# Kernel optimization log

Hardware: AMD Instinct MI355X
Metric: run time of the kernel (lower is better)

Reference implementation:

```python
import jax, jax.numpy as jnp
import numpy as np

B, C, H, W = 8, 256, 64, 64
S = 2            # area_size = sqrt(num_areas)
A = S * S        # num_areas
NH = 8           # num_heads (hardcoded in module)
EPS = 1e-5       # nn.LayerNorm default eps


def setup_inputs() -> dict:
    key = jax.random.key(0)
    ks = jax.random.split(key, 4)
    scale = 0.02
    return {
        "x": jax.random.normal(ks[0], (B, C, H, W), jnp.float32),
        "W_in": jax.random.normal(ks[1], (A, 3 * C, C), jnp.float32) * scale,
        "b_in": jnp.zeros((A, 3 * C), jnp.float32),
        "W_out": jax.random.normal(ks[2], (A, C, C), jnp.float32) * scale,
        "b_out": jnp.zeros((A, C), jnp.float32),
        "gamma": jnp.ones((C,), jnp.float32),
        "beta": jnp.zeros((C,), jnp.float32),
    }


def reference(x, W_in, b_in, W_out, b_out, gamma, beta):
    b, c, h, w = x.shape
    ah, aw = h // S, w // S
    L = ah * aw
    dh = c // NH

    # split into 2x2 areas, flatten each to a sequence: [B, A, L, C]
    # area index = i*S + j (row-major), matching the torch loop order
    xa = (x.reshape(b, c, S, ah, S, aw)
            .transpose(0, 2, 4, 3, 5, 1)   # [B, i, j, ah, aw, C]
            .reshape(b, A, L, c))

    # per-area in-projection (torch Linear: y = x @ W^T + b)
    qkv = jnp.einsum('balc,adc->bald', xa, W_in) + b_in[None, :, None, :]
    q, k, v = jnp.split(qkv, 3, axis=-1)
    q = q.reshape(b, A, L, NH, dh)
    k = k.reshape(b, A, L, NH, dh)
    v = v.reshape(b, A, L, NH, dh)

    scale = jnp.asarray(dh, x.dtype) ** -0.5
    scores = jnp.einsum('balhd,bamhd->bahlm', q * scale, k)  # [B,A,NH,L,L]
    attn = jax.nn.softmax(scores, axis=-1)
    o = jnp.einsum('bahlm,bamhd->balhd', attn, v).reshape(b, A, L, c)
    o = jnp.einsum('balc,adc->bald', o, W_out) + b_out[None, :, None, :]

    # residual + shared LayerNorm over channel dim
    y = o + xa
    mu = jnp.mean(y, axis=-1, keepdims=True)
    var = jnp.mean((y - mu) ** 2, axis=-1, keepdims=True)
    y = (y - mu) * jax.lax.rsqrt(var + EPS) * gamma + beta

    # reassemble areas back to [B, C, H, W]
    out = (y.reshape(b, S, S, ah, aw, c)
             .transpose(0, 5, 1, 3, 2, 4)  # [B, C, i, ah, j, aw]
             .reshape(b, c, h, w))
    return out
```

## Files before the change

### kernel.cpp

```cpp
#include <hip/hip_runtime.h>
#include <cstdint>
#include <cstddef>

#define B_    8
#define C_    256
#define H_    64
#define W_    64
#define A_    4
#define NH_   8
#define DH_   32
#define L_    1024
#define NPAIR 32
#define QKVN  768

typedef __bf16 bf16;
typedef __bf16 bf16x8 __attribute__((ext_vector_type(8)));
typedef __bf16 bf16x4 __attribute__((ext_vector_type(4)));
typedef float  f32x4  __attribute__((ext_vector_type(4)));

#define QSCALE 0.25506866729736328f

__device__ inline f32x4 mfma16(bf16x8 a, bf16x8 b, f32x4 c) {
    return __builtin_amdgcn_mfma_f32_16x16x32_bf16(a, b, c, 0, 0, 0);
}
__device__ inline bf16x8 ld8(const bf16* p) { return *(const bf16x8*)p; }

__device__ inline void stage16(const bf16* g, bf16* l) {
    __builtin_amdgcn_global_load_lds(
        (const __attribute__((address_space(1))) void*)g,
        (__attribute__((address_space(3))) void*)l, 16, 0, 0);
}

#define NW4 (786432 / 4)
#define NO4 (262144 / 4)
__global__ __launch_bounds__(256) void k_split(const float* __restrict__ x,
                                               bf16* __restrict__ xa,
                                               const float* __restrict__ Win,
                                               const float* __restrict__ Wout,
                                               bf16* __restrict__ Winb,
                                               bf16* __restrict__ Woutb) {
    __shared__ float lds[32][257];
    int bid = blockIdx.x;
    int t = threadIdx.x;
    if (bid >= NPAIR * 32) {
        int tid = (bid - NPAIR * 32) * 256 + t;
        if (tid < NW4) {
            float4 v = ((const float4*)Win)[tid];
            bf16x4 ov = {(bf16)v.x, (bf16)v.y, (bf16)v.z, (bf16)v.w};
            ((bf16x4*)Winb)[tid] = ov;
        } else if (tid < NW4 + NO4) {
            int t2 = tid - NW4;
            float4 v = ((const float4*)Wout)[t2];
            bf16x4 ov = {(bf16)v.x, (bf16)v.y, (bf16)v.z, (bf16)v.w};
            ((bf16x4*)Woutb)[t2] = ov;
        }
        return;
    }
    int pair = bid >> 5, p = bid & 31;
    int b = pair >> 2, a = pair & 3, i = a >> 1, j = a & 1;
    int q = t & 31, csub = t >> 5;
    const float* xb = x + (size_t)b * C_ * H_ * W_ + (size_t)(i * 32 + p) * W_ + j * 32;
    for (int r = 0; r < 32; ++r) {
        int c = r * 8 + csub;
        lds[q][c] = xb[(size_t)c * H_ * W_ + q];
    }
    __syncthreads();
    bf16* xr = xa + ((size_t)pair * L_ + (size_t)p * 32) * C_;
    for (int r = 0; r < 32; ++r) {
        xr[(size_t)r * C_ + t] = (bf16)lds[r][t];
    }
}

__global__ __launch_bounds__(256) void k_qkv(const bf16* __restrict__ xa,
                                             const bf16* __restrict__ Win,
                                             const float* __restrict__ bin,
                                             bf16* __restrict__ qk,
                                             bf16* __restrict__ vT) {
    __shared__ __align__(16) bf16 lA[128 * 64];
    __shared__ __align__(16) bf16 lB[128 * 64];
    int bid = blockIdx.x;
    int nt = bid % 6, mt = (bid / 6) & 7, pair = bid / 48;
    int a = pair & 3;
    int t = threadIdx.x, w = t >> 6, lane = t & 63;
    int wm = w >> 1, wn = w & 1;
    int quad = lane >> 4, l16 = lane & 15;
    int m0 = mt * 128, n0 = nt * 128;
    int r8 = lane >> 3, pc = lane & 7, jj = pc ^ r8;
    const bf16* ga = xa + (size_t)pair * L_ * C_ + (size_t)(m0 + w * 32 + r8) * C_ + jj * 8;
    const bf16* gb = Win + (size_t)a * QKVN * C_ + (size_t)(n0 + w * 32 + r8) * C_ + jj * 8;
    f32x4 acc[4][4];
#pragma unroll
    for (int fm = 0; fm < 4; ++fm)
#pragma unroll
        for (int fn = 0; fn < 4; ++fn) acc[fm][fn] = (f32x4){0.f, 0.f, 0.f, 0.f};
    for (int k0 = 0; k0 < C_; k0 += 64) {
        __syncthreads();
#pragma unroll
        for (int i = 0; i < 4; ++i) {
            stage16(ga + (size_t)(i * 8) * C_ + k0, lA + (w * 32 + i * 8) * 64);
            stage16(gb + (size_t)(i * 8) * C_ + k0, lB + (w * 32 + i * 8) * 64);
        }
        __syncthreads();
#pragma unroll
        for (int ks = 0; ks < 2; ++ks) {
            int p = (ks * 4 + quad) ^ (l16 & 7);
            bf16x8 am[4], bn[4];
#pragma unroll
            for (int f = 0; f < 4; ++f) {
                am[f] = *(const bf16x8*)&lA[(wm * 64 + f * 16 + l16) * 64 + p * 8];
                bn[f] = *(const bf16x8*)&lB[(wn * 64 + f * 16 + l16) * 64 + p * 8];
            }
#pragma unroll
            for (int fm = 0; fm < 4; ++fm)
#pragma unroll
                for (int fn = 0; fn < 4; ++fn)
                    acc[fm][fn] = mfma16(am[fm], bn[fn], acc[fm][fn]);
        }
    }
    int colbase = n0 + wn * 64;
    int mb = m0 + wm * 64;
    if (colbase < 512) {
        float sc = (colbase < 256) ? QSCALE : 1.0f;
        bf16* ob = qk + (size_t)pair * L_ * 512;
#pragma unroll
        for (int fn = 0; fn < 4; ++fn) {
            int col = colbase + fn * 16 + l16;
            float bias = bin[a * QKVN + col];
#pragma unroll
            for (int fm = 0; fm < 4; ++fm) {
                int m = mb + fm * 16 + quad * 4;
#pragma unroll
                for (int r = 0; r < 4; ++r)
                    ob[(size_t)(m + r) * 512 + col] = (bf16)((acc[fm][fn][r] + bias) * sc);
            }
        }
    } else {
        bf16* vb = vT + (size_t)pair * C_ * L_;
#pragma unroll
        for (int fn = 0; fn < 4; ++fn) {
            int e = colbase - 512 + fn * 16 + l16;
            float bias = bin[a * QKVN + colbase + fn * 16 + l16];
#pragma unroll
            for (int fm = 0; fm < 4; ++fm) {
                int m = mb + fm * 16 + quad * 4;
                bf16x4 pk = {(bf16)(acc[fm][fn][0] + bias), (bf16)(acc[fm][fn][1] + bias),
                             (bf16)(acc[fm][fn][2] + bias), (bf16)(acc[fm][fn][3] + bias)};
                *(bf16x4*)&vb[(size_t)e * L_ + m] = pk;
            }
        }
    }
}

__global__ __launch_bounds__(256) void k_attn(const bf16* __restrict__ qk,
                                              const bf16* __restrict__ vT,
                                              bf16* __restrict__ o) {
    __shared__ __align__(16) bf16 pl[4][4][16 * 72];
    int bid = blockIdx.x;
    int pair = bid & 31, rest = bid >> 5;
    int head = rest & 7, qb = rest >> 3;
    int t = threadIdx.x, w = t >> 6, lane = t & 63, quad = lane >> 4, l16 = lane & 15;
    const bf16* qbp  = qk + (size_t)pair * L_ * 512;
    const bf16* kptr = qbp + 256 + head * DH_ + quad * 8;
    const bf16* vt0  = vT + ((size_t)pair * C_ + head * DH_) * L_;
    int qbase = qb * 256 + w * 64;
    bf16x8 qf[4];
    f32x4 acc0[4], acc1[4], l4[4];
#pragma unroll
    for (int f = 0; f < 4; ++f) {
        qf[f] = ld8(qbp + (size_t)(qbase + f * 16 + l16) * 512 + head * DH_ + quad * 8);
        acc0[f] = (f32x4){0.f, 0.f, 0.f, 0.f};
        acc1[f] = (f32x4){0.f, 0.f, 0.f, 0.f};
        l4[f]   = (f32x4){0.f, 0.f, 0.f, 0.f};
    }
    for (int kv0 = 0; kv0 < L_; kv0 += 64) {
        bf16x8 kf[4], vf[4];
#pragma unroll
        for (int kb = 0; kb < 4; ++kb)
            kf[kb] = ld8(kptr + (size_t)(kv0 + l16 * 4 + kb) * 512);
#pragma unroll
        for (int ks = 0; ks < 2; ++ks) {
            vf[ks * 2 + 0] = ld8(vt0 + (size_t)l16 * L_ + kv0 + ks * 32 + quad * 8);
            vf[ks * 2 + 1] = ld8(vt0 + (size_t)(16 + l16) * L_ + kv0 + ks * 32 + quad * 8);
        }
#pragma unroll
        for (int f = 0; f < 4; ++f) {
            f32x4 s[4];
#pragma unroll
            for (int kb = 0; kb < 4; ++kb) s[kb] = mfma16(qf[f], kf[kb], (f32x4){0.f, 0.f, 0.f, 0.f});
            bf16* pw = &pl[w][f][0];
#pragma unroll
            for (int r = 0; r < 4; ++r) {
                float p0 = __builtin_amdgcn_exp2f(s[0][r]);
                float p1 = __builtin_amdgcn_exp2f(s[1][r]);
                float p2 = __builtin_amdgcn_exp2f(s[2][r]);
                float p3 = __builtin_amdgcn_exp2f(s[3][r]);
                l4[f][r] += (p0 + p1) + (p2 + p3);
                bf16x4 pv = {(bf16)p0, (bf16)p1, (bf16)p2, (bf16)p3};
                *(bf16x4*)&pw[(quad * 4 + r) * 72 + l16 * 4] = pv;
            }
#pragma unroll
            for (int ks = 0; ks < 2; ++ks) {
                bf16x8 pf = *(const bf16x8*)&pw[l16 * 72 + ks * 32 + quad * 8];
                acc0[f] = mfma16(pf, vf[ks * 2 + 0], acc0[f]);
                acc1[f] = mfma16(pf, vf[ks * 2 + 1], acc1[f]);
            }
        }
    }
    bf16* orow = o + (size_t)pair * L_ * C_ + head * DH_;
#pragma unroll
    for (int f = 0; f < 4; ++f) {
#pragma unroll
        for (int r = 0; r < 4; ++r) {
            float s1 = l4[f][r];
#pragma unroll
            for (int off = 1; off < 16; off <<= 1) s1 += __shfl_xor(s1, off);
            float inv = 1.f / s1;
            int row = qbase + f * 16 + quad * 4 + r;
            orow[(size_t)row * C_ + l16]      = (bf16)(acc0[f][r] * inv);
            orow[(size_t)row * C_ + 16 + l16] = (bf16)(acc1[f][r] * inv);
        }
    }
}

__global__ __launch_bounds__(256) void k_out(const bf16* __restrict__ o,
                                             const bf16* __restrict__ Wout,
                                             const float* __restrict__ bout,
                                             const bf16* __restrict__ xa,
                                             const float* __restrict__ gamma,
                                             const float* __restrict__ beta,
                                             bf16* __restrict__ y) {
    __shared__ __align__(16) bf16 lA[128 * 64];
    __shared__ __align__(16) bf16 lB[256 * 64];
    __shared__ float red[2][2][64][2];
    int bid = blockIdx.x;
    int mt = bid & 7, pair = bid >> 3;
    int a = pair & 3;
    int t = threadIdx.x, w = t >> 6, lane = t & 63;
    int wm = w >> 1, wn = w & 1;
    int quad = lane >> 4, l16 = lane & 15;
    int m0 = mt * 128;
    int r8 = lane >> 3, pc = lane & 7, jj = pc ^ r8;
    const bf16* ga = o + (size_t)pair * L_ * C_ + (size_t)(m0 + w * 32 + r8) * C_ + jj * 8;
    const bf16* gb = Wout + (size_t)a * C_ * C_ + (size_t)(w * 64 + r8) * C_ + jj * 8;
    f32x4 acc[4][8];
#pragma unroll
    for (int fm = 0; fm < 4; ++fm)
#pragma unroll
        for (int fn = 0; fn < 8; ++fn) acc[fm][fn] = (f32x4){0.f, 0.f, 0.f, 0.f};
    for (int k0 = 0; k0 < C_; k0 += 64) {
        __syncthreads();
#pragma unroll
        for (int i = 0; i < 4; ++i)
            stage16(ga + (size_t)(i * 8) * C_ + k0, lA + (w * 32 + i * 8) * 64);
#pragma unroll
        for (int i = 0; i < 8; ++i)
            stage16(gb + (size_t)(i * 8) * C_ + k0, lB + (w * 64 + i * 8) * 64);
        __syncthreads();
#pragma unroll
        for (int ks = 0; ks < 2; ++ks) {
            int p = (ks * 4 + quad) ^ (l16 & 7);
            bf16x8 am[4], bn[8];
#pragma unroll
            for (int f = 0; f < 4; ++f)
                am[f] = *(const bf16x8*)&lA[(wm * 64 + f * 16 + l16) * 64 + p * 8];
#pragma unroll
            for (int f = 0; f < 8; ++f)
                bn[f] = *(const bf16x8*)&lB[(wn * 128 + f * 16 + l16) * 64 + p * 8];
#pragma unroll
            for (int fm = 0; fm < 4; ++fm)
#pragma unroll
                for (int fn = 0; fn < 8; ++fn)
                    acc[fm][fn] = mfma16(am[fm], bn[fn], acc[fm][fn]);
        }
    }
    const bf16* xb = xa + ((size_t)pair * L_ + m0 + wm * 64) * C_;
#pragma unroll
    for (int fn = 0; fn < 8; ++fn) {
        int col = wn * 128 + fn * 16 + l16;
        float bias = bout[a * C_ + col];
#pragma unroll
        for (int fm = 0; fm < 4; ++fm)
#pragma unroll
            for (int r = 0; r < 4; ++r)
                acc[fm][fn][r] += bias + (float)xb[(size_t)(fm * 16 + quad * 4 + r) * C_ + col];
    }
#pragma unroll
    for (int fm = 0; fm < 4; ++fm) {
#pragma unroll
        for (int r = 0; r < 4; ++r) {
            float s1 = 0.f, s2 = 0.f;
#pragma unroll
            for (int fn = 0; fn < 8; ++fn) {
                float v = acc[fm][fn][r];
                s1 += v; s2 += v * v;
            }
#pragma unroll
            for (int off = 1; off < 16; off <<= 1) {
                s1 += __shfl_xor(s1, off);
                s2 += __shfl_xor(s2, off);
            }
            if (l16 == 0) {
                int rl = fm * 16 + quad * 4 + r;
                red[wm][wn][rl][0] = s1;
                red[wm][wn][rl][1] = s2;
            }
        }
    }
    __syncthreads();
    bf16* yb = y + ((size_t)pair * L_ + m0 + wm * 64) * C_;
#pragma unroll
    for (int fm = 0; fm < 4; ++fm) {
#pragma unroll
        for (int r = 0; r < 4; ++r) {
            int rl = fm * 16 + quad * 4 + r;
            float t1 = red[wm][0][rl][0] + red[wm][1][rl][0];
            float t2 = red[wm][0][rl][1] + red[wm][1][rl][1];
            float mu = t1 * (1.f / 256.f);
            float var = t2 * (1.f / 256.f) - mu * mu;
            float rstd = rsqrtf(var + 1e-5f);
#pragma unroll
            for (int fn = 0; fn < 8; ++fn) {
                int col = wn * 128 + fn * 16 + l16;
                yb[(size_t)rl * C_ + col] =
                    (bf16)((acc[fm][fn][r] - mu) * rstd * gamma[col] + beta[col]);
            }
        }
    }
}

__global__ __launch_bounds__(256) void k_merge(const bf16* __restrict__ y,
                                               float* __restrict__ out) {
    __shared__ float lds[32][257];
    int bid = blockIdx.x;
    int pair = bid >> 5, p = bid & 31;
    int b = pair >> 2, a = pair & 3, i = a >> 1, j = a & 1;
    int t = threadIdx.x;
    int q = t & 31, csub = t >> 5;
    const bf16* yr = y + ((size_t)pair * L_ + (size_t)p * 32) * C_;
    for (int r = 0; r < 32; ++r) {
        lds[r][t] = (float)yr[(size_t)r * C_ + t];
    }
    __syncthreads();
    float* xb = out + (size_t)b * C_ * H_ * W_ + (size_t)(i * 32 + p) * W_ + j * 32;
    for (int r = 0; r < 32; ++r) {
        int c = r * 8 + csub;
        xb[(size_t)c * H_ * W_ + q] = lds[q][c];
    }
}

extern "C" void kernel_launch(void* const* d_in, const int* in_sizes, int n_in,
                              void* d_out, int out_size, void* d_ws, size_t ws_size,
                              hipStream_t stream) {
    (void)in_sizes; (void)n_in; (void)out_size; (void)ws_size;
    const float* x     = (const float*)d_in[0];
    const float* Win   = (const float*)d_in[1];
    const float* bin   = (const float*)d_in[2];
    const float* Wout  = (const float*)d_in[3];
    const float* bout  = (const float*)d_in[4];
    const float* gamma = (const float*)d_in[5];
    const float* beta  = (const float*)d_in[6];
    float* out = (float*)d_out;

    char* ws = (char*)d_ws;
    bf16* xa    = (bf16*)ws;
    bf16* qk    = (bf16*)(ws + ((size_t)16 << 20));
    bf16* vT    = (bf16*)(ws + ((size_t)48 << 20));
    bf16* o     = (bf16*)(ws + ((size_t)64 << 20));
    bf16* Winb  = (bf16*)(ws + ((size_t)80 << 20));
    bf16* Woutb = (bf16*)(ws + ((size_t)82 << 20));
    bf16* y     = (bf16*)(ws + ((size_t)16 << 20));

    k_split<<<NPAIR * 32 + 1024, 256, 0, stream>>>(x, xa, Win, Wout, Winb, Woutb);
    k_qkv<<<NPAIR * 8 * 6, 256, 0, stream>>>(xa, Winb, bin, qk, vT);
    k_attn<<<NPAIR * NH_ * 4, 256, 0, stream>>>(qk, vT, o);
    k_out<<<NPAIR * 8, 256, 0, stream>>>(o, Woutb, bout, xa, gamma, beta, y);
    k_merge<<<NPAIR * 32, 256, 0, stream>>>(y, out);
}
```

Baseline: 225.7 us.

## Prefetch next K tile, split QK/exp and PV phases with sched barriers and priority

Restructures the attention inner loop. The K fragments for the next 64-key tile are now loaded after the QK/exp phase of the current tile, so the load overlaps the PV MFMAs. The QK+exp work for all four query fragments is grouped ahead of the PV MFMAs, with sched_barrier and setprio hints to order MFMA issue, and launch_bounds now requests 4 blocks per CU. The aim is to hide global load latency. In exchange it adds register pressure from the prefetched fragments and constrains the compiler's scheduling.

Measured after the change: 393.6 us. 1.74x slower.

```diff
diff --git a/kernel.cpp b/kernel.cpp
--- a/kernel.cpp
+++ b/kernel.cpp
@@ -151,9 +151,9 @@
     }
 }
 
-__global__ __launch_bounds__(256) void k_attn(const bf16* __restrict__ qk,
-                                              const bf16* __restrict__ vT,
-                                              bf16* __restrict__ o) {
+__global__ __launch_bounds__(256, 4) void k_attn(const bf16* __restrict__ qk,
+                                                 const bf16* __restrict__ vT,
+                                                 bf16* __restrict__ o) {
     __shared__ __align__(16) bf16 pl[4][4][16 * 72];
     int bid = blockIdx.x;
     int pair = bid & 31, rest = bid >> 5;
@@ -172,39 +172,61 @@
         acc1[f] = (f32x4){0.f, 0.f, 0.f, 0.f};
         l4[f]   = (f32x4){0.f, 0.f, 0.f, 0.f};
     }
+    bf16x8 ka[4], va[4];
+#pragma unroll
+    for (int kb = 0; kb < 4; ++kb)
+        ka[kb] = ld8(kptr + (size_t)(l16 * 4 + kb) * 512);
+
     for (int kv0 = 0; kv0 < L_; kv0 += 64) {
-        bf16x8 kf[4], vf[4];
-#pragma unroll
-        for (int kb = 0; kb < 4; ++kb)
-            kf[kb] = ld8(kptr + (size_t)(kv0 + l16 * 4 + kb) * 512);
 #pragma unroll
         for (int ks = 0; ks < 2; ++ks) {
-            vf[ks * 2 + 0] = ld8(vt0 + (size_t)l16 * L_ + kv0 + ks * 32 + quad * 8);
-            vf[ks * 2 + 1] = ld8(vt0 + (size_t)(16 + l16) * L_ + kv0 + ks * 32 + quad * 8);
-        }
+            va[ks * 2 + 0] = ld8(vt0 + (size_t)l16 * L_ + kv0 + ks * 32 + quad * 8);
+            va[ks * 2 + 1] = ld8(vt0 + (size_t)(16 + l16) * L_ + kv0 + ks * 32 + quad * 8);
+        }
+        __builtin_amdgcn_sched_barrier(0);
 #pragma unroll
         for (int f = 0; f < 4; ++f) {
             f32x4 s[4];
-#pragma unroll
-            for (int kb = 0; kb < 4; ++kb) s[kb] = mfma16(qf[f], kf[kb], (f32x4){0.f, 0.f, 0.f, 0.f});
+            __builtin_amdgcn_s_setprio(1);
+#pragma unroll
+            for (int kb = 0; kb < 4; ++kb)
+                s[kb] = mfma16(qf[f], ka[kb], (f32x4){0.f, 0.f, 0.f, 0.f});
+            __builtin_amdgcn_s_setprio(0);
+            f32x4 e0, e1, e2, e3;
+#pragma unroll
+            for (int r = 0; r < 4; ++r) {
+                e0[r] = __builtin_amdgcn_exp2f(s[0][r]);
+                e1[r] = __builtin_amdgcn_exp2f(s[1][r]);
+                e2[r] = __builtin_amdgcn_exp2f(s[2][r]);
+                e3[r] = __builtin_amdgcn_exp2f(s[3][r]);
+            }
+            l4[f] += (e0 + e1) + (e2 + e3);
             bf16* pw = &pl[w][f][0];
 #pragma unroll
             for (int r = 0; r < 4; ++r) {
-                float p0 = __builtin_amdgcn_exp2f(s[0][r]);
-                float p1 = __builtin_amdgcn_exp2f(s[1][r]);
-                float p2 = __builtin_amdgcn_exp2f(s[2][r]);
-                float p3 = __builtin_amdgcn_exp2f(s[3][r]);
-                l4[f][r] += (p0 + p1) + (p2 + p3);
-                bf16x4 pv = {(bf16)p0, (bf16)p1, (bf16)p2, (bf16)p3};
+                bf16x4 pv = {(bf16)e0[r], (bf16)e1[r], (bf16)e2[r], (bf16)e3[r]};
                 *(bf16x4*)&pw[(quad * 4 + r) * 72 + l16 * 4] = pv;
             }
+        }
+        __builtin_amdgcn_sched_barrier(0);
+        if (kv0 + 64 < L_) {
+#pragma unroll
+            for (int kb = 0; kb < 4; ++kb)
+                ka[kb] = ld8(kptr + (size_t)(kv0 + 64 + l16 * 4 + kb) * 512);
+        }
+        __builtin_amdgcn_sched_barrier(0);
+        __builtin_amdgcn_s_setprio(1);
+#pragma unroll
+        for (int f = 0; f < 4; ++f) {
+            const bf16* pw = &pl[w][f][0];
 #pragma unroll
             for (int ks = 0; ks < 2; ++ks) {
                 bf16x8 pf = *(const bf16x8*)&pw[l16 * 72 + ks * 32 + quad * 8];
-                acc0[f] = mfma16(pf, vf[ks * 2 + 0], acc0[f]);
-                acc1[f] = mfma16(pf, vf[ks * 2 + 1], acc1[f]);
-            }
-        }
+                acc0[f] = mfma16(pf, va[ks * 2 + 0], acc0[f]);
+                acc1[f] = mfma16(pf, va[ks * 2 + 1], acc1[f]);
+            }
+        }
+        __builtin_amdgcn_s_setprio(0);
     }
     bf16* orow = o + (size_t)pair * L_ * C_ + head * DH_;
 #pragma unroll
```

## Stage shared K/V tiles in LDS with prefetch and swizzle P buffer

Applied to the files above, without the earlier changes.

The attention kernel now loads each 64-key K and V tile cooperatively into LDS once per block instead of every wave issuing its own redundant global loads. The next tile is prefetched right after the current one is read into registers, with block-wide barriers around the loop. The P scratch buffer changes from a padded layout to an XOR-swizzled one to avoid bank conflicts. Together these aim to cut global memory traffic and LDS conflicts, at the cost of two __syncthreads per iteration and extra LDS use that may lower occupancy.

New measurement: 212.1 us. 1.06x faster.

```diff
diff --git a/kernel.cpp b/kernel.cpp
--- a/kernel.cpp
+++ b/kernel.cpp
@@ -154,14 +154,19 @@
 __global__ __launch_bounds__(256) void k_attn(const bf16* __restrict__ qk,
                                               const bf16* __restrict__ vT,
                                               bf16* __restrict__ o) {
-    __shared__ __align__(16) bf16 pl[4][4][16 * 72];
+    __shared__ __align__(16) bf16 pl[4][4][1024];
+    __shared__ __align__(16) bf16 klds[4 * 512];
+    __shared__ __align__(16) bf16 vlds[4 * 512];
     int bid = blockIdx.x;
     int pair = bid & 31, rest = bid >> 5;
     int head = rest & 7, qb = rest >> 3;
     int t = threadIdx.x, w = t >> 6, lane = t & 63, quad = lane >> 4, l16 = lane & 15;
-    const bf16* qbp  = qk + (size_t)pair * L_ * 512;
-    const bf16* kptr = qbp + 256 + head * DH_ + quad * 8;
-    const bf16* vt0  = vT + ((size_t)pair * C_ + head * DH_) * L_;
+    const bf16* qbp = qk + (size_t)pair * L_ * 512;
+    const bf16* kg = qbp + (size_t)(l16 * 4 + w) * 512 + 256 + head * DH_ + quad * 8;
+    const bf16* vg = vT + ((size_t)pair * C_ + head * DH_ + (w & 1) * 16 + l16) * L_
+                        + (w >> 1) * 32 + quad * 8;
+    bf16* kdst = &klds[w * 512];
+    bf16* vdst = &vlds[w * 512];
     int qbase = qb * 256 + w * 64;
     bf16x8 qf[4];
     f32x4 acc0[4], acc1[4], l4[4];
@@ -172,22 +177,28 @@
         acc1[f] = (f32x4){0.f, 0.f, 0.f, 0.f};
         l4[f]   = (f32x4){0.f, 0.f, 0.f, 0.f};
     }
+    stage16(kg, kdst);
+    stage16(vg, vdst);
+    __syncthreads();
+
     for (int kv0 = 0; kv0 < L_; kv0 += 64) {
         bf16x8 kf[4], vf[4];
 #pragma unroll
-        for (int kb = 0; kb < 4; ++kb)
-            kf[kb] = ld8(kptr + (size_t)(kv0 + l16 * 4 + kb) * 512);
-#pragma unroll
-        for (int ks = 0; ks < 2; ++ks) {
-            vf[ks * 2 + 0] = ld8(vt0 + (size_t)l16 * L_ + kv0 + ks * 32 + quad * 8);
-            vf[ks * 2 + 1] = ld8(vt0 + (size_t)(16 + l16) * L_ + kv0 + ks * 32 + quad * 8);
-        }
+        for (int i = 0; i < 4; ++i) {
+            kf[i] = ld8(&klds[(i * 64 + lane) * 8]);
+            vf[i] = ld8(&vlds[(i * 64 + lane) * 8]);
+        }
+        __syncthreads();
+        int kvn = (kv0 + 64) & (L_ - 1);
+        stage16(kg + (size_t)kvn * 512, kdst);
+        stage16(vg + kvn, vdst);
 #pragma unroll
         for (int f = 0; f < 4; ++f) {
             f32x4 s[4];
 #pragma unroll
-            for (int kb = 0; kb < 4; ++kb) s[kb] = mfma16(qf[f], kf[kb], (f32x4){0.f, 0.f, 0.f, 0.f});
-            bf16* pw = &pl[w][f][0];
+            for (int kb = 0; kb < 4; ++kb)
+                s[kb] = mfma16(qf[f], kf[kb], (f32x4){0.f, 0.f, 0.f, 0.f});
+            char* pw = (char*)&pl[w][f][0];
 #pragma unroll
             for (int r = 0; r < 4; ++r) {
                 float p0 = __builtin_amdgcn_exp2f(s[0][r]);
@@ -196,15 +207,19 @@
                 float p3 = __builtin_amdgcn_exp2f(s[3][r]);
                 l4[f][r] += (p0 + p1) + (p2 + p3);
                 bf16x4 pv = {(bf16)p0, (bf16)p1, (bf16)p2, (bf16)p3};
-                *(bf16x4*)&pw[(quad * 4 + r) * 72 + l16 * 4] = pv;
+                int row = quad * 4 + r;
+                int wo = (row * 128 + l16 * 8) ^ ((row & 7) << 4);
+                *(bf16x4*)(pw + wo) = pv;
             }
 #pragma unroll
             for (int ks = 0; ks < 2; ++ks) {
-                bf16x8 pf = *(const bf16x8*)&pw[l16 * 72 + ks * 32 + quad * 8];
+                int ro = (l16 * 128 + ks * 64 + quad * 16) ^ ((l16 & 7) << 4);
+                bf16x8 pf = *(const bf16x8*)(pw + ro);
                 acc0[f] = mfma16(pf, vf[ks * 2 + 0], acc0[f]);
                 acc1[f] = mfma16(pf, vf[ks * 2 + 1], acc1[f]);
             }
         }
+        __syncthreads();
     }
     bf16* orow = o + (size_t)pair * L_ * C_ + head * DH_;
 #pragma unroll
```
